# Kernel optimization log

Measured on AMD Instinct MI355X. Metric: run time of the kernel, lower is better.

## Reference

```python
import jax, jax.numpy as jnp
import numpy as np

MS_KS = 9
C = 256
BN_EPS = 1e-5


def setup_inputs() -> dict:
    key = jax.random.key(0)
    k1, k2, k3 = jax.random.split(key, 3)
    p2_r = jax.random.normal(k1, (2, C, 64, 128), dtype=jnp.float32)
    conv_w = jax.random.normal(k2, (C, C, 1, MS_KS), dtype=jnp.float32) * 0.02
    conv1_w = jax.random.normal(k3, (1, C, 1, 1), dtype=jnp.float32) * 0.05
    bn_gamma = jnp.ones((1,), jnp.float32)
    bn_beta = jnp.zeros((1,), jnp.float32)
    return dict(p2_r=p2_r, conv_w=conv_w, conv1_w=conv1_w,
                bn_gamma=bn_gamma, bn_beta=bn_beta)


def _scnn_pass(x, M):
    # x: [b,c,h,w]. Each step applies conv(1,ms_ks) to a width-1 column with
    # zero padding ms_ks//2 -> only the center tap contributes, i.e. a 256x256
    # channel matmul per column, followed by relu and residual add.
    cols = jnp.moveaxis(x, 3, 0)  # [w,b,c,h]
    def step(carry, col):
        new = col + jax.nn.relu(jnp.einsum('oc,bch->boh', M, carry))
        return new, new
    _, outs = jax.lax.scan(step, cols[0], cols[1:])
    outs = jnp.concatenate([cols[:1], outs], axis=0)[::-1]  # mirrors out[::-1]
    return jnp.moveaxis(outs, 0, 3)


def _upsample_bilinear_ac(x, factor=4):
    # F.interpolate(mode='bilinear', align_corners=True)
    b, c, h, w = x.shape
    Ho, Wo = factor * h, factor * w
    ys = jnp.arange(Ho, dtype=x.dtype) * ((h - 1) / (Ho - 1))
    xs = jnp.arange(Wo, dtype=x.dtype) * ((w - 1) / (Wo - 1))
    y0 = jnp.floor(ys).astype(jnp.int32)
    y1 = jnp.minimum(y0 + 1, h - 1)
    wy = (ys - y0.astype(x.dtype))[None, None, :, None]
    rows = x[:, :, y0, :] * (1 - wy) + x[:, :, y1, :] * wy  # [b,c,Ho,w]
    x0 = jnp.floor(xs).astype(jnp.int32)
    x1 = jnp.minimum(x0 + 1, w - 1)
    wx = (xs - x0.astype(x.dtype))[None, None, None, :]
    return rows[:, :, :, x0] * (1 - wx) + rows[:, :, :, x1] * wx


def reference(p2_r, conv_w, conv1_w, bn_gamma, bn_beta):
    M = conv_w[:, :, 0, MS_KS // 2]  # center tap, [c_out, c_in]
    x = _scnn_pass(p2_r, M)                     # reverse=False
    x = _scnn_pass(x[:, :, :, ::-1], M)         # reverse=True (slices[::-1])
    x = _upsample_bilinear_ac(x, 4)             # [b,256,4h,4w]
    x = jnp.einsum('oc,bchw->bohw', conv1_w[:, :, 0, 0], x)  # 1x1 conv -> 1 ch
    # BatchNorm2d(1), training-mode batch statistics (biased variance)
    mean = jnp.mean(x, axis=(0, 2, 3), keepdims=True)
    var = jnp.mean((x - mean) ** 2, axis=(0, 2, 3), keepdims=True)
    x = (x - mean) * jax.lax.rsqrt(var + BN_EPS)
    x = x * bn_gamma[None, :, None, None] + bn_beta[None, :, None, None]
    return jax.nn.sigmoid(x)
```

## Files before the change

kernel.cpp:

```cpp
#include <hip/hip_runtime.h>


typedef _Float16 f16x8 __attribute__((ext_vector_type(8)));
typedef _Float16 f16x4 __attribute__((ext_vector_type(4)));
typedef float    f32x4 __attribute__((ext_vector_type(4)));

static __device__ __forceinline__ void sync_lds() {
  asm volatile("s_waitcnt lgkmcnt(0)" ::: "memory");
  __builtin_amdgcn_s_barrier();
  asm volatile("" ::: "memory");
}

static __device__ __forceinline__ float dpp_even(float v) {
  int t = __builtin_bit_cast(int, v);
  t = __builtin_amdgcn_update_dpp(t, t, 0xA0, 0xF, 0xF, false);
  return __builtin_bit_cast(float, t);
}

extern "C" __global__ void k_extract(const float* __restrict__ convw,
                                     _Float16* __restrict__ Md) {
  int q = blockIdx.x * 256 + threadIdx.x;
  float4 v = ((const float4*)convw)[q];
  float vv[4] = {v.x, v.y, v.z, v.w};
  int f = q * 4;
#pragma unroll
  for (int e = 0; e < 4; ++e) {
    int flat = f + e;
    if (flat % 9 == 4) Md[flat / 9] = (_Float16)vv[e];
  }
}

struct SM {
  _Float16 cy[2][256];
  _Float16 pad_[32];
  _Float16 zh[128 * 256];
};

extern "C" __global__ void __launch_bounds__(256, 1)
k_scan(const float* __restrict__ p2, const _Float16* __restrict__ Md,
       const float* __restrict__ conv1, float* __restrict__ sout,
       float* __restrict__ stats) {
  __shared__ SM sm;
  const int tid  = threadIdx.x;
  const int l    = tid & 63;
  const int r    = tid >> 6;
  const int col  = l & 15;
  const int quad = l >> 4;
  const int b    = blockIdx.x >> 6;
  const int h    = blockIdx.x & 63;

  if (blockIdx.x == 0 && tid == 0) { stats[0] = 0.f; stats[1] = 0.f; }

  const bool isY   = (col == 0);
  const bool isZ   = (col == 1);
  const bool zlane = (l & 1);

  int mrow[4];
#pragma unroll
  for (int t = 0; t < 4; ++t) mrow[t] = (r * 4 + t) * 16 + quad * 4;

  f16x8 A[4][8];
#pragma unroll
  for (int t = 0; t < 4; ++t)
#pragma unroll
    for (int ch = 0; ch < 8; ++ch)
      A[t][ch] = *(const f16x8*)(Md + ((r*4+t)*16 + col) * 256 + ch*32 + quad*8);

  const float* pbase = p2 + (size_t)b * 2097152 + (size_t)h * 128;

  if (isY) {
#pragma unroll
    for (int t = 0; t < 4; ++t) {
      f16x4 p;
#pragma unroll
      for (int i = 0; i < 4; ++i)
        p[i] = (_Float16)pbase[(size_t)(mrow[t] + i) * 8192];
      *(f16x4*)(sm.cy[0] + mrow[t]) = p;
      *(f16x4*)(sm.zh    + mrow[t]) = p;
    }
  }

  float cc[4][4], cn[4][4];
  if (isY) {
#pragma unroll
    for (int t = 0; t < 4; ++t)
#pragma unroll
      for (int i = 0; i < 4; ++i) {
        cc[t][i] = pbase[(size_t)(mrow[t] + i) * 8192 + 1];
        cn[t][i] = pbase[(size_t)(mrow[t] + i) * 8192 + 2];
      }
  }
  sync_lds();

  const _Float16* pY0 = sm.cy[0] + quad * 8;
  const _Float16* pY1 = sm.cy[1] + quad * 8;
  const _Float16* zrd = sm.zh + quad * 8;
  _Float16*       zwr = sm.zh + 256;

#define STEP(W, PY, WY, C)                                                     \
  do {                                                                         \
    const _Float16* bsrc = zlane ? zrd : (PY);                                 \
    f16x8 B[8];                                                                \
    _Pragma("unroll")                                                          \
    for (int ch = 0; ch < 8; ++ch)                                             \
      B[ch] = *(const f16x8*)(bsrc + ch * 32);                                 \
    f32x4 a0[4], a1[4];                                                        \
    _Pragma("unroll")                                                          \
    for (int t = 0; t < 4; ++t) {                                              \
      a0[t] = (f32x4){0.f, 0.f, 0.f, 0.f};                                     \
      a1[t] = (f32x4){0.f, 0.f, 0.f, 0.f};                                     \
    }                                                                          \
    _Pragma("unroll")                                                          \
    for (int ch = 0; ch < 4; ++ch) {                                           \
      _Pragma("unroll")                                                        \
      for (int t = 0; t < 4; ++t) {                                            \
        a0[t] = __builtin_amdgcn_mfma_f32_16x16x32_f16(A[t][ch],   B[ch],   a0[t],0,0,0); \
        a1[t] = __builtin_amdgcn_mfma_f32_16x16x32_f16(A[t][ch+4], B[ch+4], a1[t],0,0,0); \
      }                                                                        \
    }                                                                          \
    f32x4 acc[4];                                                              \
    _Pragma("unroll")                                                          \
    for (int t = 0; t < 4; ++t) acc[t] = a0[t] + a1[t];                        \
    f32x4 yf[4] = {};                                                          \
    if (isY) {                                                                 \
      _Pragma("unroll")                                                        \
      for (int t = 0; t < 4; ++t) {                                            \
        f16x4 yh;                                                              \
        _Pragma("unroll")                                                      \
        for (int i = 0; i < 4; ++i) {                                          \
          yf[t][i] = (C)[t][i] + fmaxf(acc[t][i], 0.f);                        \
          yh[i] = (_Float16)yf[t][i];                                          \
        }                                                                      \
        *(f16x4*)((WY) + mrow[t]) = yh;                                        \
      }                                                                        \
      if ((W) + 2 < 128) {                                                     \
        _Pragma("unroll")                                                      \
        for (int t = 0; t < 4; ++t)                                            \
          _Pragma("unroll")                                                    \
          for (int i = 0; i < 4; ++i)                                          \
            (C)[t][i] = pbase[(size_t)(mrow[t] + i) * 8192 + (W) + 2];         \
      }                                                                        \
    }                                                                          \
    _Pragma("unroll")                                                          \
    for (int t = 0; t < 4; ++t)                                                \
      _Pragma("unroll")                                                        \
      for (int i = 0; i < 4; ++i)                                              \
        yf[t][i] = dpp_even(yf[t][i]);                                         \
    if (isZ) {                                                                 \
      _Pragma("unroll")                                                        \
      for (int t = 0; t < 4; ++t) {                                            \
        f16x4 zo;                                                              \
        _Pragma("unroll")                                                      \
        for (int i = 0; i < 4; ++i)                                            \
          zo[i] = (_Float16)(yf[t][i] + fmaxf(acc[t][i], 0.f));                \
        *(f16x4*)(zwr + mrow[t]) = zo;                                         \
      }                                                                        \
    }                                                                          \
    zrd += 256; zwr += 256;                                                    \
    sync_lds();                                                                \
  } while (0)

#pragma unroll 1
  for (int w = 1; w < 127; w += 2) {
    STEP(w,     pY0, sm.cy[1], cc);
    STEP(w + 1, pY1, sm.cy[0], cn);
  }
  STEP(127, pY0, sm.cy[1], cc);
#undef STEP

  {
    const int w    = tid >> 1;
    const int part = tid & 1;
    const _Float16* zr = sm.zh + w * 256 + part * 128;
    const float*    vr = conv1 + part * 128;
    float s = 0.f;
#pragma unroll
    for (int j = 0; j < 16; ++j) {
      f16x8 zv = *(const f16x8*)(zr + j * 8);
      float4 v0 = *(const float4*)(vr + j * 8);
      float4 v1 = *(const float4*)(vr + j * 8 + 4);
      s += v0.x * (float)zv[0] + v0.y * (float)zv[1]
         + v0.z * (float)zv[2] + v0.w * (float)zv[3]
         + v1.x * (float)zv[4] + v1.y * (float)zv[5]
         + v1.z * (float)zv[6] + v1.w * (float)zv[7];
    }
    s += __shfl_xor(s, 1, 64);
    if (part == 0) sout[(blockIdx.x << 7) + (127 - w)] = s;
  }
}

static __device__ __forceinline__ float bilin(const float* __restrict__ s,
                                              int idx) {
  int bb  = idx >> 17;
  int rem = idx & 131071;
  int ho  = rem >> 9;
  int wo  = rem & 511;
  const float SY = 63.0f / 255.0f, SX = 127.0f / 511.0f;
  float fy = (float)ho * SY;
  int y0 = (int)fy; int y1 = min(y0 + 1, 63); float wy = fy - (float)y0;
  float fx = (float)wo * SX;
  int x0 = (int)fx; int x1 = min(x0 + 1, 127); float wx = fx - (float)x0;
  const float* sb = s + bb * 8192;
  float cA = sb[y0 * 128 + x0] * (1.f - wy) + sb[y1 * 128 + x0] * wy;
  float cB = sb[y0 * 128 + x1] * (1.f - wy) + sb[y1 * 128 + x1] * wy;
  return cA * (1.f - wx) + cB * wx;
}

extern "C" __global__ void k_stats(const float* __restrict__ s,
                                   float* __restrict__ stats) {
  int tid  = threadIdx.x;
  int base = blockIdx.x * 1024 + tid;
  float sum = 0.f, ssq = 0.f;
#pragma unroll
  for (int i = 0; i < 4; ++i) {
    float u = bilin(s, base + i * 256);
    sum += u; ssq += u * u;
  }
#pragma unroll
  for (int off = 32; off > 0; off >>= 1) {
    sum += __shfl_xor(sum, off, 64);
    ssq += __shfl_xor(ssq, off, 64);
  }
  __shared__ float ls[4], lq[4];
  int wv = tid >> 6;
  if ((tid & 63) == 0) { ls[wv] = sum; lq[wv] = ssq; }
  __syncthreads();
  if (tid == 0) {
    atomicAdd(&stats[0], ls[0] + ls[1] + ls[2] + ls[3]);
    atomicAdd(&stats[1], lq[0] + lq[1] + lq[2] + lq[3]);
  }
}

extern "C" __global__ void k_norm(const float* __restrict__ s,
                                  const float* __restrict__ stats,
                                  const float* __restrict__ gamma,
                                  const float* __restrict__ beta,
                                  float* __restrict__ out) {
  int tid  = threadIdx.x;
  int base = blockIdx.x * 1024 + tid;
  const float invN = 1.f / 262144.f;
  float mean  = stats[0] * invN;
  float var   = stats[1] * invN - mean * mean;
  float scale = rsqrtf(var + 1e-5f) * gamma[0];
  float bias  = beta[0] - mean * scale;
#pragma unroll
  for (int i = 0; i < 4; ++i) {
    int idx = base + i * 256;
    float u = bilin(s, idx);
    float x = u * scale + bias;
    out[idx] = 1.f / (1.f + __expf(-x));
  }
}

extern "C" void kernel_launch(void* const* d_in, const int* in_sizes, int n_in,
                              void* d_out, int out_size, void* d_ws, size_t ws_size,
                              hipStream_t stream) {
  const float* p2    = (const float*)d_in[0];
  const float* convw = (const float*)d_in[1];
  const float* conv1 = (const float*)d_in[2];
  const float* gamma = (const float*)d_in[3];
  const float* beta  = (const float*)d_in[4];
  float* out = (float*)d_out;

  char* ws = (char*)d_ws;
  float*    s     = (float*)ws;
  float*    stats = (float*)(ws + 65536);
  _Float16* Md    = (_Float16*)(ws + 65792);

  hipLaunchKernelGGL(k_extract, dim3(576), dim3(256), 0, stream, convw, Md);
  hipLaunchKernelGGL(k_scan,    dim3(128), dim3(256), 0, stream, p2, Md, conv1, s, stats);
  hipLaunchKernelGGL(k_stats,   dim3(256), dim3(256), 0, stream, s, stats);
  hipLaunchKernelGGL(k_norm,    dim3(256), dim3(256), 0, stream, s, stats, gamma, beta, out);
}
```

Before: 202.2 us.

## Pair two scan rows per block and ping-pong MFMA with elementwise phases

Each block now runs two independent (b,h) scan chains in two 4-wave groups. While one group does the MFMA matmul phase, the other does the relu/residual/store phase, so the tensor-core and VALU/LDS latency of the serial chain can overlap. The 1x1 conv projection is accumulated on the fly into small per-step partial sums, which removes the full 128x256 fp16 history buffer in LDS. The weight extraction kernel is dropped and the center tap is gathered directly from conv_w with strided loads. The trade-offs are twice as many barriers per step and only 64 blocks.

```diff
diff --git a/kernel.cpp b/kernel.cpp
--- a/kernel.cpp
+++ b/kernel.cpp
@@ -17,40 +17,35 @@
   return __builtin_bit_cast(float, t);
 }
 
-extern "C" __global__ void k_extract(const float* __restrict__ convw,
-                                     _Float16* __restrict__ Md) {
-  int q = blockIdx.x * 256 + threadIdx.x;
-  float4 v = ((const float4*)convw)[q];
-  float vv[4] = {v.x, v.y, v.z, v.w};
-  int f = q * 4;
-#pragma unroll
-  for (int e = 0; e < 4; ++e) {
-    int flat = f + e;
-    if (flat % 9 == 4) Md[flat / 9] = (_Float16)vv[e];
-  }
-}
-
-struct SM {
-  _Float16 cy[2][256];
-  _Float16 pad_[32];
-  _Float16 zh[128 * 256];
+struct GSM {
+  _Float16 cy[256];
+  _Float16 pad0[32];
+  _Float16 cz[256];
+  _Float16 pad1[32];
+  float    sp[128 * 16];
 };
-
-extern "C" __global__ void __launch_bounds__(256, 1)
-k_scan(const float* __restrict__ p2, const _Float16* __restrict__ Md,
+struct SM { GSM g[2]; };
+
+extern "C" __global__ void __launch_bounds__(512, 2)
+k_scan(const float* __restrict__ p2, const float* __restrict__ convw,
        const float* __restrict__ conv1, float* __restrict__ sout,
        float* __restrict__ stats) {
   __shared__ SM sm;
   const int tid  = threadIdx.x;
   const int l    = tid & 63;
-  const int r    = tid >> 6;
+  const int wv   = tid >> 6;
+  const int g    = wv >> 2;
+  const int r    = wv & 3;
+  const bool gA  = (g == 0);
   const int col  = l & 15;
   const int quad = l >> 4;
-  const int b    = blockIdx.x >> 6;
-  const int h    = blockIdx.x & 63;
+  const int gh   = blockIdx.x * 2 + g;
+  const int b    = gh >> 6;
+  const int h    = gh & 63;
 
   if (blockIdx.x == 0 && tid == 0) { stats[0] = 0.f; stats[1] = 0.f; }
 
+  GSM& S = sm.g[g];
   const bool isY   = (col == 0);
   const bool isZ   = (col == 1);
   const bool zlane = (l & 1);
@@ -61,66 +56,90 @@
 
   f16x8 A[4][8];
 #pragma unroll
-  for (int t = 0; t < 4; ++t)
+  for (int t = 0; t < 4; ++t) {
+    const float* wrow = convw + (size_t)((r * 4 + t) * 16 + col) * 2304 + 4;
 #pragma unroll
     for (int ch = 0; ch < 8; ++ch)
-      A[t][ch] = *(const f16x8*)(Md + ((r*4+t)*16 + col) * 256 + ch*32 + quad*8);
+#pragma unroll
+      for (int j = 0; j < 8; ++j)
+        A[t][ch][j] = (_Float16)wrow[(ch * 32 + quad * 8 + j) * 9];
+  }
 
   const float* pbase = p2 + (size_t)b * 2097152 + (size_t)h * 128;
 
-  if (isY) {
-#pragma unroll
-    for (int t = 0; t < 4; ++t) {
-      f16x4 p;
-#pragma unroll
-      for (int i = 0; i < 4; ++i)
-        p[i] = (_Float16)pbase[(size_t)(mrow[t] + i) * 8192];
-      *(f16x4*)(sm.cy[0] + mrow[t]) = p;
-      *(f16x4*)(sm.zh    + mrow[t]) = p;
+  float c_vv[4][4], c_ev[4][4];
+
+  {
+    if (isY || isZ) {
+      float c0[4][4];
+#pragma unroll
+      for (int t = 0; t < 4; ++t)
+#pragma unroll
+        for (int i = 0; i < 4; ++i)
+          c0[t][i] = pbase[(size_t)(mrow[t] + i) * 8192];
+      if (isY) {
+#pragma unroll
+        for (int t = 0; t < 4; ++t) {
+          f16x4 p;
+#pragma unroll
+          for (int i = 0; i < 4; ++i) p[i] = (_Float16)c0[t][i];
+          *(f16x4*)(S.cy + mrow[t]) = p;
+          *(f16x4*)(S.cz + mrow[t]) = p;
+        }
+      } else {
+        float p = 0.f;
+#pragma unroll
+        for (int t = 0; t < 4; ++t)
+#pragma unroll
+          for (int i = 0; i < 4; ++i) {
+            c_vv[t][i] = conv1[mrow[t] + i];
+            p += c_vv[t][i] * c0[t][i];
+          }
+        S.sp[0 * 16 + r * 4 + quad] = p;
+      }
     }
-  }
-
-  float cc[4][4], cn[4][4];
-  if (isY) {
-#pragma unroll
-    for (int t = 0; t < 4; ++t)
-#pragma unroll
-      for (int i = 0; i < 4; ++i) {
-        cc[t][i] = pbase[(size_t)(mrow[t] + i) * 8192 + 1];
-        cn[t][i] = pbase[(size_t)(mrow[t] + i) * 8192 + 2];
-      }
-  }
-  sync_lds();
-
-  const _Float16* pY0 = sm.cy[0] + quad * 8;
-  const _Float16* pY1 = sm.cy[1] + quad * 8;
-  const _Float16* zrd = sm.zh + quad * 8;
-  _Float16*       zwr = sm.zh + 256;
-
-#define STEP(W, PY, WY, C)                                                     \
+    if (isY) {
+#pragma unroll
+      for (int t = 0; t < 4; ++t)
+#pragma unroll
+        for (int i = 0; i < 4; ++i) {
+          c_vv[t][i] = pbase[(size_t)(mrow[t] + i) * 8192 + 1];
+          c_ev[t][i] = pbase[(size_t)(mrow[t] + i) * 8192 + 2];
+        }
+    }
+  }
+  sync_lds();
+
+  const _Float16* bsrc = (zlane ? S.cz : S.cy) + quad * 8;
+
+  f32x4 acc0[4], acc1[4];
+
+#define RM()                                                                   \
   do {                                                                         \
-    const _Float16* bsrc = zlane ? zrd : (PY);                                 \
     f16x8 B[8];                                                                \
     _Pragma("unroll")                                                          \
     for (int ch = 0; ch < 8; ++ch)                                             \
       B[ch] = *(const f16x8*)(bsrc + ch * 32);                                 \
-    f32x4 a0[4], a1[4];                                                        \
     _Pragma("unroll")                                                          \
     for (int t = 0; t < 4; ++t) {                                              \
-      a0[t] = (f32x4){0.f, 0.f, 0.f, 0.f};                                     \
-      a1[t] = (f32x4){0.f, 0.f, 0.f, 0.f};                                     \
+      acc0[t] = (f32x4){0.f, 0.f, 0.f, 0.f};                                   \
+      acc1[t] = (f32x4){0.f, 0.f, 0.f, 0.f};                                   \
     }                                                                          \
     _Pragma("unroll")                                                          \
     for (int ch = 0; ch < 4; ++ch) {                                           \
       _Pragma("unroll")                                                        \
       for (int t = 0; t < 4; ++t) {                                            \
-        a0[t] = __builtin_amdgcn_mfma_f32_16x16x32_f16(A[t][ch],   B[ch],   a0[t],0,0,0); \
-        a1[t] = __builtin_amdgcn_mfma_f32_16x16x32_f16(A[t][ch+4], B[ch+4], a1[t],0,0,0); \
-      }                                                                        \
-    }                                                                          \
+        acc0[t] = __builtin_amdgcn_mfma_f32_16x16x32_f16(A[t][ch],   B[ch],   acc0[t],0,0,0); \
+        acc1[t] = __builtin_amdgcn_mfma_f32_16x16x32_f16(A[t][ch+4], B[ch+4], acc1[t],0,0,0); \
+      }                                                                        \
+    }                                                                          \
+  } while (0)
+
+#define EW(W, C)                                                               \
+  do {                                                                         \
     f32x4 acc[4];                                                              \
     _Pragma("unroll")                                                          \
-    for (int t = 0; t < 4; ++t) acc[t] = a0[t] + a1[t];                        \
+    for (int t = 0; t < 4; ++t) acc[t] = acc0[t] + acc1[t];                    \
     f32x4 yf[4] = {};                                                          \
     if (isY) {                                                                 \
       _Pragma("unroll")                                                        \
@@ -131,7 +150,7 @@
           yf[t][i] = (C)[t][i] + fmaxf(acc[t][i], 0.f);                        \
           yh[i] = (_Float16)yf[t][i];                                          \
         }                                                                      \
-        *(f16x4*)((WY) + mrow[t]) = yh;                                        \
+        *(f16x4*)(S.cy + mrow[t]) = yh;                                        \
       }                                                                        \
       if ((W) + 2 < 128) {                                                     \
         _Pragma("unroll")                                                      \
@@ -147,45 +166,53 @@
       for (int i = 0; i < 4; ++i)                                              \
         yf[t][i] = dpp_even(yf[t][i]);                                         \
     if (isZ) {                                                                 \
+      float p = 0.f;                                                           \
       _Pragma("unroll")                                                        \
       for (int t = 0; t < 4; ++t) {                                            \
         f16x4 zo;                                                              \
         _Pragma("unroll")                                                      \
-        for (int i = 0; i < 4; ++i)                                            \
-          zo[i] = (_Float16)(yf[t][i] + fmaxf(acc[t][i], 0.f));                \
-        *(f16x4*)(zwr + mrow[t]) = zo;                                         \
-      }                                                                        \
-    }                                                                          \
-    zrd += 256; zwr += 256;                                                    \
-    sync_lds();                                                                \
+        for (int i = 0; i < 4; ++i) {                                          \
+          float z = yf[t][i] + fmaxf(acc[t][i], 0.f);                          \
+          zo[i] = (_Float16)z;                                                 \
+          p += c_vv[t][i] * z;                                                 \
+        }                                                                      \
+        *(f16x4*)(S.cz + mrow[t]) = zo;                                        \
+      }                                                                        \
+      S.sp[(W) * 16 + r * 4 + quad] = p;                                       \
+    }                                                                          \
   } while (0)
 
 #pragma unroll 1
   for (int w = 1; w < 127; w += 2) {
-    STEP(w,     pY0, sm.cy[1], cc);
-    STEP(w + 1, pY1, sm.cy[0], cn);
-  }
-  STEP(127, pY0, sm.cy[1], cc);
-#undef STEP
+    if (gA) RM(); else if (w > 1) EW(w - 1, c_ev);
+    sync_lds();
+    if (gA) EW(w, c_vv); else RM();
+    sync_lds();
+    if (gA) RM(); else EW(w, c_vv);
+    sync_lds();
+    if (gA) EW(w + 1, c_ev); else RM();
+    sync_lds();
+  }
+  if (gA) RM(); else EW(126, c_ev);
+  sync_lds();
+  if (gA) EW(127, c_vv); else RM();
+  sync_lds();
+  if (!gA) EW(127, c_vv);
+  sync_lds();
+#undef RM
+#undef EW
 
   {
-    const int w    = tid >> 1;
+    const int rg   = tid >> 8;
+    const int w    = (tid >> 1) & 127;
     const int part = tid & 1;
-    const _Float16* zr = sm.zh + w * 256 + part * 128;
-    const float*    vr = conv1 + part * 128;
-    float s = 0.f;
-#pragma unroll
-    for (int j = 0; j < 16; ++j) {
-      f16x8 zv = *(const f16x8*)(zr + j * 8);
-      float4 v0 = *(const float4*)(vr + j * 8);
-      float4 v1 = *(const float4*)(vr + j * 8 + 4);
-      s += v0.x * (float)zv[0] + v0.y * (float)zv[1]
-         + v0.z * (float)zv[2] + v0.w * (float)zv[3]
-         + v1.x * (float)zv[4] + v1.y * (float)zv[5]
-         + v1.z * (float)zv[6] + v1.w * (float)zv[7];
-    }
+    const float* q = sm.g[rg].sp + w * 16 + part * 8;
+    float4 t0 = *(const float4*)q;
+    float4 t1 = *(const float4*)(q + 4);
+    float s = t0.x + t0.y + t0.z + t0.w + t1.x + t1.y + t1.z + t1.w;
     s += __shfl_xor(s, 1, 64);
-    if (part == 0) sout[(blockIdx.x << 7) + (127 - w)] = s;
+    if (part == 0)
+      sout[((blockIdx.x * 2 + rg) << 7) + (127 - w)] = s;
   }
 }
 
@@ -265,10 +292,8 @@
   char* ws = (char*)d_ws;
   float*    s     = (float*)ws;
   float*    stats = (float*)(ws + 65536);
-  _Float16* Md    = (_Float16*)(ws + 65792);
-
-  hipLaunchKernelGGL(k_extract, dim3(576), dim3(256), 0, stream, convw, Md);
-  hipLaunchKernelGGL(k_scan,    dim3(128), dim3(256), 0, stream, p2, Md, conv1, s, stats);
-  hipLaunchKernelGGL(k_stats,   dim3(256), dim3(256), 0, stream, s, stats);
-  hipLaunchKernelGGL(k_norm,    dim3(256), dim3(256), 0, stream, s, stats, gamma, beta, out);
-}
+
+  hipLaunchKernelGGL(k_scan,  dim3(64),  dim3(512), 0, stream, p2, convw, conv1, s, stats);
+  hipLaunchKernelGGL(k_stats, dim3(256), dim3(256), 0, stream, s, stats);
+  hipLaunchKernelGGL(k_norm,  dim3(256), dim3(256), 0, stream, s, stats, gamma, beta, out);
+}
```

Result: slower. 406.2 us (+100.9%).

## Ping-pong two scan rows per block, overlapping MFMA with elementwise phases

Applied to the files above, without the earlier changes.

Each block now runs two independent (batch, row) scans in two 4-wave groups, each with its own LDS buffers. The groups alternate phases, so one runs the matrix multiply while the other runs the relu/residual/store epilogue, with a barrier between phases. This is meant to hide the epilogue behind MFMA work while halving the block count. It also merges the two split accumulator chains into one 8-deep MFMA chain, which lengthens the dependency latency, and it doubles the number of barriers per column step.

```diff
diff --git a/kernel.cpp b/kernel.cpp
--- a/kernel.cpp
+++ b/kernel.cpp
@@ -30,27 +30,33 @@
   }
 }
 
-struct SM {
-  _Float16 cy[2][256];
-  _Float16 pad_[32];
+struct GSM {
+  _Float16 cy[256];
+  _Float16 pad0[32];
   _Float16 zh[128 * 256];
 };
-
-extern "C" __global__ void __launch_bounds__(256, 1)
+struct SM { GSM g[2]; };
+
+extern "C" __global__ void __launch_bounds__(512, 1)
 k_scan(const float* __restrict__ p2, const _Float16* __restrict__ Md,
        const float* __restrict__ conv1, float* __restrict__ sout,
        float* __restrict__ stats) {
   __shared__ SM sm;
   const int tid  = threadIdx.x;
   const int l    = tid & 63;
-  const int r    = tid >> 6;
+  const int wv   = tid >> 6;
+  const int g    = wv >> 2;
+  const int r    = wv & 3;
+  const bool gA  = (g == 0);
   const int col  = l & 15;
   const int quad = l >> 4;
-  const int b    = blockIdx.x >> 6;
-  const int h    = blockIdx.x & 63;
+  const int gh   = blockIdx.x * 2 + g;
+  const int b    = gh >> 6;
+  const int h    = gh & 63;
 
   if (blockIdx.x == 0 && tid == 0) { stats[0] = 0.f; stats[1] = 0.f; }
 
+  GSM& S = sm.g[g];
   const bool isY   = (col == 0);
   const bool isZ   = (col == 1);
   const bool zlane = (l & 1);
@@ -75,8 +81,8 @@
 #pragma unroll
       for (int i = 0; i < 4; ++i)
         p[i] = (_Float16)pbase[(size_t)(mrow[t] + i) * 8192];
-      *(f16x4*)(sm.cy[0] + mrow[t]) = p;
-      *(f16x4*)(sm.zh    + mrow[t]) = p;
+      *(f16x4*)(S.cy + mrow[t]) = p;
+      *(f16x4*)(S.zh + mrow[t]) = p;
     }
   }
 
@@ -92,35 +98,32 @@
   }
   sync_lds();
 
-  const _Float16* pY0 = sm.cy[0] + quad * 8;
-  const _Float16* pY1 = sm.cy[1] + quad * 8;
-  const _Float16* zrd = sm.zh + quad * 8;
-  _Float16*       zwr = sm.zh + 256;
-
-#define STEP(W, PY, WY, C)                                                     \
+  const _Float16* pY  = S.cy + quad * 8;
+  const _Float16* zrd = S.zh + quad * 8;
+  _Float16*       zwr = S.zh + 256;
+
+  f32x4 acc[4];
+
+#define RM()                                                                   \
   do {                                                                         \
-    const _Float16* bsrc = zlane ? zrd : (PY);                                 \
+    const _Float16* bs = zlane ? zrd : pY;                                     \
     f16x8 B[8];                                                                \
     _Pragma("unroll")                                                          \
     for (int ch = 0; ch < 8; ++ch)                                             \
-      B[ch] = *(const f16x8*)(bsrc + ch * 32);                                 \
-    f32x4 a0[4], a1[4];                                                        \
-    _Pragma("unroll")                                                          \
-    for (int t = 0; t < 4; ++t) {                                              \
-      a0[t] = (f32x4){0.f, 0.f, 0.f, 0.f};                                     \
-      a1[t] = (f32x4){0.f, 0.f, 0.f, 0.f};                                     \
+      B[ch] = *(const f16x8*)(bs + ch * 32);                                   \
+    _Pragma("unroll")                                                          \
+    for (int t = 0; t < 4; ++t) acc[t] = (f32x4){0.f, 0.f, 0.f, 0.f};          \
+    _Pragma("unroll")                                                          \
+    for (int ch = 0; ch < 8; ++ch) {                                           \
+      _Pragma("unroll")                                                        \
+      for (int t = 0; t < 4; ++t)                                              \
+        acc[t] = __builtin_amdgcn_mfma_f32_16x16x32_f16(A[t][ch], B[ch], acc[t],0,0,0); \
     }                                                                          \
-    _Pragma("unroll")                                                          \
-    for (int ch = 0; ch < 4; ++ch) {                                           \
-      _Pragma("unroll")                                                        \
-      for (int t = 0; t < 4; ++t) {                                            \
-        a0[t] = __builtin_amdgcn_mfma_f32_16x16x32_f16(A[t][ch],   B[ch],   a0[t],0,0,0); \
-        a1[t] = __builtin_amdgcn_mfma_f32_16x16x32_f16(A[t][ch+4], B[ch+4], a1[t],0,0,0); \
-      }                                                                        \
-    }                                                                          \
-    f32x4 acc[4];                                                              \
-    _Pragma("unroll")                                                          \
-    for (int t = 0; t < 4; ++t) acc[t] = a0[t] + a1[t];                        \
+    zrd += 256;                                                                \
+  } while (0)
+
+#define EW(W, C)                                                               \
+  do {                                                                         \
     f32x4 yf[4] = {};                                                          \
     if (isY) {                                                                 \
       _Pragma("unroll")                                                        \
@@ -131,7 +134,7 @@
           yf[t][i] = (C)[t][i] + fmaxf(acc[t][i], 0.f);                        \
           yh[i] = (_Float16)yf[t][i];                                          \
         }                                                                      \
-        *(f16x4*)((WY) + mrow[t]) = yh;                                        \
+        *(f16x4*)(S.cy + mrow[t]) = yh;                                        \
       }                                                                        \
       if ((W) + 2 < 128) {                                                     \
         _Pragma("unroll")                                                      \
@@ -156,22 +159,34 @@
         *(f16x4*)(zwr + mrow[t]) = zo;                                         \
       }                                                                        \
     }                                                                          \
-    zrd += 256; zwr += 256;                                                    \
-    sync_lds();                                                                \
+    zwr += 256;                                                                \
   } while (0)
 
 #pragma unroll 1
   for (int w = 1; w < 127; w += 2) {
-    STEP(w,     pY0, sm.cy[1], cc);
-    STEP(w + 1, pY1, sm.cy[0], cn);
-  }
-  STEP(127, pY0, sm.cy[1], cc);
-#undef STEP
+    if (gA) RM(); else { if (w > 1) EW(w - 1, cn); }
+    sync_lds();
+    if (gA) EW(w, cc); else RM();
+    sync_lds();
+    if (gA) RM(); else EW(w, cc);
+    sync_lds();
+    if (gA) EW(w + 1, cn); else RM();
+    sync_lds();
+  }
+  if (gA) RM(); else EW(126, cn);
+  sync_lds();
+  if (gA) EW(127, cc); else RM();
+  sync_lds();
+  if (!gA) EW(127, cc);
+  sync_lds();
+#undef RM
+#undef EW
 
   {
-    const int w    = tid >> 1;
+    const int rg   = tid >> 8;
+    const int w    = (tid >> 1) & 127;
     const int part = tid & 1;
-    const _Float16* zr = sm.zh + w * 256 + part * 128;
+    const _Float16* zr = sm.g[rg].zh + w * 256 + part * 128;
     const float*    vr = conv1 + part * 128;
     float s = 0.f;
 #pragma unroll
@@ -185,7 +200,8 @@
          + v1.z * (float)zv[6] + v1.w * (float)zv[7];
     }
     s += __shfl_xor(s, 1, 64);
-    if (part == 0) sout[(blockIdx.x << 7) + (127 - w)] = s;
+    if (part == 0)
+      sout[((blockIdx.x * 2 + rg) << 7) + (127 - w)] = s;
   }
 }
 
@@ -268,7 +284,7 @@
   _Float16* Md    = (_Float16*)(ws + 65792);
 
   hipLaunchKernelGGL(k_extract, dim3(576), dim3(256), 0, stream, convw, Md);
-  hipLaunchKernelGGL(k_scan,    dim3(128), dim3(256), 0, stream, p2, Md, conv1, s, stats);
+  hipLaunchKernelGGL(k_scan,    dim3(64),  dim3(512), 0, stream, p2, Md, conv1, s, stats);
   hipLaunchKernelGGL(k_stats,   dim3(256), dim3(256), 0, stream, s, stats);
   hipLaunchKernelGGL(k_norm,    dim3(256), dim3(256), 0, stream, s, stats, gamma, beta, out);
 }
```

Result: slower. 273.1 us (+35.0%).
